# Kernel tuning notes

Measured on AMD Instinct MI355X. Metric: run time of the kernel, lower is better.

The kernel has to match this reference:

```python
import jax, jax.numpy as jnp
import numpy as np

N_NODES = 50000


def gcn_conv(x, W, b, src, dst, n_nodes):
    """PyG GCNConv: add self-loops, symmetric norm, linear, scatter-add, bias."""
    h = x @ W  # [N, out]
    # degree with self-loops: deg[i] = 1 + (# edges with dst == i)
    deg = 1.0 + jax.ops.segment_sum(jnp.ones_like(dst, dtype=h.dtype), dst,
                                    num_segments=n_nodes)
    dinv = jax.lax.rsqrt(deg)  # deg^{-1/2}
    # per-edge norm for non-self-loop edges
    norm = dinv[src] * dinv[dst]  # [E]
    agg = jax.ops.segment_sum(h[src] * norm[:, None], dst,
                              num_segments=n_nodes)
    # self-loop contribution: dinv[i]*dinv[i]*h[i] = h[i]/deg[i]
    agg = agg + h * (dinv * dinv)[:, None]
    return agg + b


def setup_inputs() -> dict:
    key = jax.random.key(0)
    ks = jax.random.split(key, 6)
    x = jax.random.normal(ks[0], (N_NODES, 512), dtype=jnp.float32)
    edge_index = jax.random.randint(ks[1], (2, 800000), 0, N_NODES,
                                    dtype=jnp.int64)
    W1 = jax.random.normal(ks[2], (512, 256), dtype=jnp.float32) * (512 ** -0.5)
    b1 = jnp.zeros((256,), dtype=jnp.float32)
    W2 = jax.random.normal(ks[3], (256, 256), dtype=jnp.float32) * (256 ** -0.5)
    b2 = jnp.zeros((256,), dtype=jnp.float32)
    W3 = jax.random.normal(ks[4], (256, 64), dtype=jnp.float32) * (256 ** -0.5)
    b3 = jnp.zeros((64,), dtype=jnp.float32)
    return {"x": x, "edge_index": edge_index, "W1": W1, "b1": b1,
            "W2": W2, "b2": b2, "W3": W3, "b3": b3}


def reference(x, edge_index, W1, b1, W2, b2, W3, b3):
    src, dst = edge_index[0], edge_index[1]
    n = x.shape[0]
    h = gcn_conv(x, W1, b1, src, dst, n)
    h = jax.nn.relu(h)  # dropout is a no-op in eval mode
    h = gcn_conv(h, W2, b2, src, dst, n)
    h = jax.nn.relu(h)
    h = gcn_conv(h, W3, b3, src, dst, n)
    # faithful to the original: softmax then log_softmax
    h = jax.nn.softmax(h, axis=1)
    return jax.nn.log_softmax(h, axis=1)
```

## Files before the change

kernel.cpp:

```cpp
#include <hip/hip_runtime.h>
#include <cstdint>
#include <cstddef>

typedef float  f32x4  __attribute__((ext_vector_type(4)));
typedef __bf16 bf16x8 __attribute__((ext_vector_type(8)));
typedef unsigned short u16x8 __attribute__((ext_vector_type(8)));
typedef unsigned short u16x4 __attribute__((ext_vector_type(4)));

__device__ __forceinline__ unsigned short f2bf(float f) {
  union { float f; unsigned int u; } v; v.f = f;
  unsigned int r = v.u + 0x7fffu + ((v.u >> 16) & 1u);
  return (unsigned short)(r >> 16);
}
__device__ __forceinline__ float bf2f(unsigned short h) {
  union { unsigned int u; float f; } v; v.u = ((unsigned int)h) << 16;
  return v.f;
}

__device__ __forceinline__ void async_copy16(const unsigned short* g, unsigned short* l) {
  __builtin_amdgcn_global_load_lds(
      (const __attribute__((address_space(1))) unsigned int*)g,
      (__attribute__((address_space(3))) unsigned int*)l, 16, 0, 0);
}

#define NN 50000
#define MPAD 50048
#define SCAN_BLOCKS 196

#define XB_BLOCKS 12512
#define ZB_BLOCKS 196
#define WB_BLOCKS 104

__global__ __launch_bounds__(256) void gcn_prep_k(
    const float* __restrict__ X, unsigned short* __restrict__ xb,
    int* __restrict__ cnt,
    const float* __restrict__ W1, const float* __restrict__ W2,
    const float* __restrict__ W3,
    unsigned short* __restrict__ W1T, unsigned short* __restrict__ W2T,
    unsigned short* __restrict__ W3T) {
  int b = blockIdx.x;
  if (b < XB_BLOCKS) {
    int idx8 = (b * 256 + threadIdx.x) * 8;
    int row = idx8 >> 9;
    u16x8 o;
    if (row < NN) {
      const float* s = &X[idx8];
      float4 v0 = *(const float4*)s;
      float4 v1 = *(const float4*)(s + 4);
      o[0] = f2bf(v0.x); o[1] = f2bf(v0.y); o[2] = f2bf(v0.z); o[3] = f2bf(v0.w);
      o[4] = f2bf(v1.x); o[5] = f2bf(v1.y); o[6] = f2bf(v1.z); o[7] = f2bf(v1.w);
    } else {
      o = u16x8{0, 0, 0, 0, 0, 0, 0, 0};
    }
    *(u16x8*)&xb[idx8] = o;
  } else if (b < XB_BLOCKS + ZB_BLOCKS) {
    int i = (b - XB_BLOCKS) * 256 + threadIdx.x;
    if (i < NN) cnt[i] = 0;
  } else if (b < XB_BLOCKS + ZB_BLOCKS + WB_BLOCKS) {
    int idx8 = ((b - XB_BLOCKS - ZB_BLOCKS) * 256 + threadIdx.x) * 8;
    u16x8 o;
    if (idx8 < 131072) {
#pragma unroll
      for (int j = 0; j < 8; j++) {
        int idx = idx8 + j; int n = idx >> 9, k = idx & 511;
        o[j] = f2bf(W1[(size_t)k * 256 + n]);
      }
      *(u16x8*)&W1T[idx8] = o;
    } else if (idx8 < 196608) {
      int j0 = idx8 - 131072;
#pragma unroll
      for (int j = 0; j < 8; j++) {
        int idx = j0 + j; int n = idx >> 8, k = idx & 255;
        o[j] = f2bf(W2[(size_t)k * 256 + n]);
      }
      *(u16x8*)&W2T[j0] = o;
    } else if (idx8 < 212992) {
      int j0 = idx8 - 196608;
#pragma unroll
      for (int j = 0; j < 8; j++) {
        int idx = j0 + j; int n = idx >> 8, k = idx & 255;
        o[j] = f2bf(W3[(size_t)k * 64 + n]);
      }
      *(u16x8*)&W3T[j0] = o;
    }
  }
}

__global__ void gcn_count_k(const int* __restrict__ dst, int* __restrict__ cnt, int E) {
  int e = blockIdx.x * 256 + threadIdx.x;
  if (e < E) atomicAdd(&cnt[dst[e]], 1);
}

__global__ __launch_bounds__(256) void gcn_scan_blocks_k(
    const int* __restrict__ cnt, int* __restrict__ blockSum, int nNodes) {
  __shared__ int sw[4];
  int t = threadIdx.x;
  int i = blockIdx.x * 256 + t;
  int v = (i < nNodes) ? cnt[i] : 0;
  for (int off = 32; off > 0; off >>= 1) v += __shfl_down(v, off);
  if ((t & 63) == 0) sw[t >> 6] = v;
  __syncthreads();
  if (t == 0) blockSum[blockIdx.x] = sw[0] + sw[1] + sw[2] + sw[3];
}

__global__ __launch_bounds__(256) void gcn_scan_tops_k(
    int* __restrict__ blockSum, int nBlocks) {
  __shared__ int sb[256];
  int t = threadIdx.x;
  int v = (t < nBlocks) ? blockSum[t] : 0;
  sb[t] = v;
  __syncthreads();
  for (int off = 1; off < 256; off <<= 1) {
    int x = (t >= off) ? sb[t - off] : 0;
    __syncthreads();
    sb[t] += x;
    __syncthreads();
  }
  if (t < nBlocks) blockSum[t] = sb[t] - v;
}

__global__ __launch_bounds__(256) void gcn_scan_final_k(
    const int* __restrict__ cnt, const int* __restrict__ blockSum,
    int* __restrict__ rs, int* __restrict__ cur, float* __restrict__ dinv,
    int nNodes, int E) {
  __shared__ int sb[256];
  int t = threadIdx.x;
  int i = blockIdx.x * 256 + t;
  int v = (i < nNodes) ? cnt[i] : 0;
  sb[t] = v;
  __syncthreads();
  for (int off = 1; off < 256; off <<= 1) {
    int x = (t >= off) ? sb[t - off] : 0;
    __syncthreads();
    sb[t] += x;
    __syncthreads();
  }
  if (i < nNodes) {
    int off = blockSum[blockIdx.x] + sb[t] - v;
    rs[i] = off; cur[i] = off;
    dinv[i] = rsqrtf(1.0f + (float)v);
  }
  if (i == 0) rs[nNodes] = E;
}

__global__ void gcn_scatter_k(const int* __restrict__ src, const int* __restrict__ dst,
                              int* __restrict__ cur, const float* __restrict__ dinv,
                              int2* __restrict__ e2, int E) {
  int e = blockIdx.x * 256 + threadIdx.x;
  if (e < E) {
    int d = dst[e];
    int s = src[e];
    int p = atomicAdd(&cur[d], 1);
    int2 v; v.x = s; v.y = __float_as_int(dinv[s] * dinv[d]);
    e2[p] = v;
  }
}

template<int BN, int WTN>
__global__ __launch_bounds__(256) void gcn_gemm_k(
    const unsigned short* __restrict__ A,
    const unsigned short* __restrict__ Bt,
    unsigned short* __restrict__ C,
    int K, int N) {
  __shared__ __align__(16) unsigned short lds_a[128 * 32];
  __shared__ __align__(16) unsigned short lds_b[BN * 32];
  const int t = threadIdx.x;
  const int wave = t >> 6, lane = t & 63;
  const int wr = wave >> 1, wc = wave & 1;
  const int quad = lane >> 4, lrow = lane & 15;
  const int m0 = blockIdx.x * 128;
  const int n0 = blockIdx.y * BN;

  f32x4 acc[4][WTN] = {};

  for (int k0 = 0; k0 < K; k0 += 32) {
    __syncthreads();
    for (int q = t; q < 512; q += 256) {
      int r = q >> 2, c = (q & 3) * 8;
      async_copy16(&A[(size_t)(m0 + r) * K + k0 + c], &lds_a[q * 8]);
    }
    for (int q = t; q < BN * 4; q += 256) {
      int r = q >> 2, c = (q & 3) * 8;
      async_copy16(&Bt[(size_t)(n0 + r) * K + k0 + c], &lds_b[q * 8]);
    }
    __syncthreads();
    bf16x8 af[4], bfr[WTN];
#pragma unroll
    for (int mt = 0; mt < 4; mt++)
      af[mt] = *(const bf16x8*)&lds_a[(wr * 64 + mt * 16 + lrow) * 32 + quad * 8];
#pragma unroll
    for (int nt = 0; nt < WTN; nt++)
      bfr[nt] = *(const bf16x8*)&lds_b[(wc * (BN / 2) + nt * 16 + lrow) * 32 + quad * 8];
#pragma unroll
    for (int mt = 0; mt < 4; mt++)
#pragma unroll
      for (int nt = 0; nt < WTN; nt++)
        acc[mt][nt] = __builtin_amdgcn_mfma_f32_16x16x32_bf16(af[mt], bfr[nt], acc[mt][nt], 0, 0, 0);
  }

#pragma unroll
  for (int mt = 0; mt < 4; mt++)
#pragma unroll
    for (int nt = 0; nt < WTN; nt++)
#pragma unroll
      for (int r = 0; r < 4; r++) {
        int row = m0 + wr * 64 + mt * 16 + quad * 4 + r;
        int col = n0 + wc * (BN / 2) + nt * 16 + lrow;
        C[(size_t)row * N + col] = f2bf(acc[mt][nt][r]);
      }
}

template<int D>
__global__ __launch_bounds__(256) void gcn_agg_relu_k(
    const unsigned short* __restrict__ h, const int* __restrict__ rs,
    const int2* __restrict__ e2, const float* __restrict__ dinv,
    const float* __restrict__ bias, unsigned short* __restrict__ out, int nNodes) {
  int wave = threadIdx.x >> 6, lane = threadIdx.x & 63;
  int i = blockIdx.x * 4 + wave;
  if (i >= nNodes) return;
  int half = lane >> 5, sub = lane & 31;
  int f0 = sub * 8;
  float di = dinv[i];
  u16x8 hv = *(const u16x8*)&h[(size_t)i * D + f0];
  float wself = (half == 0) ? di * di : 0.0f;
  float acc[8];
#pragma unroll
  for (int j = 0; j < 8; j++) acc[j] = bf2f(hv[j]) * wself;

  int e0 = rs[i], e1 = rs[i + 1];
  int nIter = (e1 - e0 + 7) >> 3;
  int e = e0 + half;
  for (int k = 0; k < nIter; k++) {
    int idx[4]; float w[4];
#pragma unroll
    for (int u = 0; u < 4; u++) {
      int ee = e + 2 * u;
      bool v = ee < e1;
      int2 pr = e2[v ? ee : e0];
      idx[u] = v ? pr.x : i;
      w[u] = v ? __int_as_float(pr.y) : 0.0f;
    }
    u16x8 r0 = *(const u16x8*)&h[(size_t)idx[0] * D + f0];
    u16x8 r1 = *(const u16x8*)&h[(size_t)idx[1] * D + f0];
    u16x8 r2 = *(const u16x8*)&h[(size_t)idx[2] * D + f0];
    u16x8 r3 = *(const u16x8*)&h[(size_t)idx[3] * D + f0];
#pragma unroll
    for (int j = 0; j < 8; j++)
      acc[j] += bf2f(r0[j]) * w[0] + bf2f(r1[j]) * w[1] +
                bf2f(r2[j]) * w[2] + bf2f(r3[j]) * w[3];
    e += 8;
  }
#pragma unroll
  for (int j = 0; j < 8; j++) acc[j] += __shfl_xor(acc[j], 32);
  if (half == 0) {
    u16x8 o;
#pragma unroll
    for (int j = 0; j < 8; j++) {
      float r = acc[j] + bias[f0 + j];
      o[j] = f2bf(r > 0.0f ? r : 0.0f);
    }
    *(u16x8*)&out[(size_t)i * D + f0] = o;
  }
}

__global__ __launch_bounds__(256) void gcn_agg_final_k(
    const unsigned short* __restrict__ h, const int* __restrict__ rs,
    const int2* __restrict__ e2, const float* __restrict__ dinv,
    const float* __restrict__ bias, float* __restrict__ out, int nNodes) {
  int wave = threadIdx.x >> 6, lane = threadIdx.x & 63;
  int i = blockIdx.x * 4 + wave;
  if (i >= nNodes) return;
  int qtr = lane >> 4, sub = lane & 15;
  int f0 = sub * 4;
  float di = dinv[i];
  u16x4 hv = *(const u16x4*)&h[(size_t)i * 64 + f0];
  float wself = (qtr == 0) ? di * di : 0.0f;
  float acc[4];
#pragma unroll
  for (int j = 0; j < 4; j++) acc[j] = bf2f(hv[j]) * wself;

  int e0 = rs[i], e1 = rs[i + 1];
  int nIter = (e1 - e0 + 7) >> 3;
  int e = e0 + qtr;
  for (int k = 0; k < nIter; k++) {
    int idx[2]; float w[2];
#pragma unroll
    for (int u = 0; u < 2; u++) {
      int ee = e + 4 * u;
      bool v = ee < e1;
      int2 pr = e2[v ? ee : e0];
      idx[u] = v ? pr.x : i;
      w[u] = v ? __int_as_float(pr.y) : 0.0f;
    }
    u16x4 r0 = *(const u16x4*)&h[(size_t)idx[0] * 64 + f0];
    u16x4 r1 = *(const u16x4*)&h[(size_t)idx[1] * 64 + f0];
#pragma unroll
    for (int j = 0; j < 4; j++)
      acc[j] += bf2f(r0[j]) * w[0] + bf2f(r1[j]) * w[1];
    e += 8;
  }
#pragma unroll
  for (int j = 0; j < 4; j++) {
    acc[j] += __shfl_xor(acc[j], 16);
    acc[j] += __shfl_xor(acc[j], 32);
    acc[j] += bias[f0 + j];
  }
  float m = fmaxf(fmaxf(acc[0], acc[1]), fmaxf(acc[2], acc[3]));
#pragma unroll
  for (int off = 8; off > 0; off >>= 1) m = fmaxf(m, __shfl_xor(m, off));
  float ex[4], s = 0.0f;
#pragma unroll
  for (int j = 0; j < 4; j++) { ex[j] = __expf(acc[j] - m); s += ex[j]; }
#pragma unroll
  for (int off = 8; off > 0; off >>= 1) s += __shfl_xor(s, off);
  float rcs = 1.0f / s;
  float p[4], s2 = 0.0f;
#pragma unroll
  for (int j = 0; j < 4; j++) { p[j] = ex[j] * rcs; s2 += __expf(p[j]); }
#pragma unroll
  for (int off = 8; off > 0; off >>= 1) s2 += __shfl_xor(s2, off);
  float ls = __logf(s2);
  if (qtr == 0) {
    float4 o; o.x = p[0] - ls; o.y = p[1] - ls; o.z = p[2] - ls; o.w = p[3] - ls;
    *(float4*)&out[(size_t)i * 64 + f0] = o;
  }
}

extern "C" void kernel_launch(void* const* d_in, const int* in_sizes, int n_in,
                              void* d_out, int out_size, void* d_ws, size_t ws_size,
                              hipStream_t stream) {
  const float* x    = (const float*)d_in[0];
  const int*   eidx = (const int*)d_in[1];
  const float* W1   = (const float*)d_in[2];
  const float* b1   = (const float*)d_in[3];
  const float* W2   = (const float*)d_in[4];
  const float* b2   = (const float*)d_in[5];
  const float* W3   = (const float*)d_in[6];
  const float* b3   = (const float*)d_in[7];
  float* out = (float*)d_out;

  const int E = in_sizes[1] / 2;
  const int* src = eidx;
  const int* dst = eidx + E;

  char* p = (char*)d_ws;
  auto alloc = [&](size_t bytes) -> void* {
    void* r = (void*)p;
    p += (bytes + 255) & ~(size_t)255;
    return r;
  };
  unsigned short* xb  = (unsigned short*)alloc((size_t)MPAD * 512 * 2);
  unsigned short* hb  = (unsigned short*)alloc((size_t)MPAD * 256 * 2);
  unsigned short* ab  = (unsigned short*)alloc((size_t)MPAD * 256 * 2);
  unsigned short* h3  = (unsigned short*)alloc((size_t)MPAD * 64 * 2);
  unsigned short* W1T = (unsigned short*)alloc((size_t)256 * 512 * 2);
  unsigned short* W2T = (unsigned short*)alloc((size_t)256 * 256 * 2);
  unsigned short* W3T = (unsigned short*)alloc((size_t)64 * 256 * 2);
  int*   cnt  = (int*)alloc((size_t)NN * 4);
  int*   rs   = (int*)alloc((size_t)(NN + 1) * 4);
  int*   cur  = (int*)alloc((size_t)NN * 4);
  float* dinv = (float*)alloc((size_t)NN * 4);
  int2*  e2   = (int2*)alloc((size_t)E * 8);
  int*   bsum = (int*)alloc((size_t)SCAN_BLOCKS * 4);

  gcn_prep_k<<<XB_BLOCKS + ZB_BLOCKS + WB_BLOCKS, 256, 0, stream>>>(
      x, xb, cnt, W1, W2, W3, W1T, W2T, W3T);
  gcn_count_k<<<(E + 255) / 256, 256, 0, stream>>>(dst, cnt, E);
  gcn_scan_blocks_k<<<SCAN_BLOCKS, 256, 0, stream>>>(cnt, bsum, NN);
  gcn_scan_tops_k<<<1, 256, 0, stream>>>(bsum, SCAN_BLOCKS);
  gcn_scan_final_k<<<SCAN_BLOCKS, 256, 0, stream>>>(cnt, bsum, rs, cur, dinv, NN, E);
  gcn_scatter_k<<<(E + 255) / 256, 256, 0, stream>>>(src, dst, cur, dinv, e2, E);

  const int MB = MPAD / 128;
  gcn_gemm_k<128, 4><<<dim3(MB, 2), 256, 0, stream>>>(xb, W1T, hb, 512, 256);
  gcn_agg_relu_k<256><<<(NN + 3) / 4, 256, 0, stream>>>(hb, rs, e2, dinv, b1, ab, NN);
  gcn_gemm_k<128, 4><<<dim3(MB, 2), 256, 0, stream>>>(ab, W2T, hb, 256, 256);
  gcn_agg_relu_k<256><<<(NN + 3) / 4, 256, 0, stream>>>(hb, rs, e2, dinv, b2, ab, NN);
  gcn_gemm_k<64, 2><<<dim3(MB, 1), 256, 0, stream>>>(ab, W3T, h3, 256, 64);
  gcn_agg_final_k<<<(NN + 3) / 4, 256, 0, stream>>>(h3, rs, e2, dinv, b3, out, NN);

  (void)n_in; (void)out_size; (void)ws_size;
}
```

Before: 466.6 us.

## Store GEMM outputs as FP8 to halve gather traffic in aggregation

```diff
diff --git a/kernel.cpp b/kernel.cpp
--- a/kernel.cpp
+++ b/kernel.cpp
@@ -3,6 +3,7 @@
 #include <cstddef>
 
 typedef float  f32x4  __attribute__((ext_vector_type(4)));
+typedef float  f32x2  __attribute__((ext_vector_type(2)));
 typedef __bf16 bf16x8 __attribute__((ext_vector_type(8)));
 typedef unsigned short u16x8 __attribute__((ext_vector_type(8)));
 typedef unsigned short u16x4 __attribute__((ext_vector_type(4)));
@@ -16,6 +17,22 @@
   union { unsigned int u; float f; } v; v.u = ((unsigned int)h) << 16;
   return v.f;
 }
+__device__ __forceinline__ unsigned char f2fp8(float f) {
+  return (unsigned char)(__builtin_amdgcn_cvt_pk_fp8_f32(f, f, 0, false) & 0xff);
+}
+__device__ __forceinline__ void fp8x8_to_f32(uint2 d, float* f) {
+  f32x2 a = __builtin_amdgcn_cvt_pk_f32_fp8((int)d.x, false);
+  f32x2 b = __builtin_amdgcn_cvt_pk_f32_fp8((int)d.x, true);
+  f32x2 c = __builtin_amdgcn_cvt_pk_f32_fp8((int)d.y, false);
+  f32x2 e = __builtin_amdgcn_cvt_pk_f32_fp8((int)d.y, true);
+  f[0] = a.x; f[1] = a.y; f[2] = b.x; f[3] = b.y;
+  f[4] = c.x; f[5] = c.y; f[6] = e.x; f[7] = e.y;
+}
+__device__ __forceinline__ void fp8x4_to_f32(unsigned int d, float* f) {
+  f32x2 a = __builtin_amdgcn_cvt_pk_f32_fp8((int)d, false);
+  f32x2 b = __builtin_amdgcn_cvt_pk_f32_fp8((int)d, true);
+  f[0] = a.x; f[1] = a.y; f[2] = b.x; f[3] = b.y;
+}
 
 __device__ __forceinline__ void async_copy16(const unsigned short* g, unsigned short* l) {
   __builtin_amdgcn_global_load_lds(
@@ -28,16 +45,20 @@
 #define SCAN_BLOCKS 196
 
 #define XB_BLOCKS 12512
-#define ZB_BLOCKS 196
 #define WB_BLOCKS 104
+
+__global__ void gcn_zero_k(int* __restrict__ p, int n) {
+  int i = blockIdx.x * 256 + threadIdx.x;
+  if (i < n) p[i] = 0;
+}
 
 __global__ __launch_bounds__(256) void gcn_prep_k(
     const float* __restrict__ X, unsigned short* __restrict__ xb,
-    int* __restrict__ cnt,
     const float* __restrict__ W1, const float* __restrict__ W2,
     const float* __restrict__ W3,
     unsigned short* __restrict__ W1T, unsigned short* __restrict__ W2T,
-    unsigned short* __restrict__ W3T) {
+    unsigned short* __restrict__ W3T,
+    const int* __restrict__ dst, int* __restrict__ cnt, int E) {
   int b = blockIdx.x;
   if (b < XB_BLOCKS) {
     int idx8 = (b * 256 + threadIdx.x) * 8;
@@ -53,11 +74,8 @@
       o = u16x8{0, 0, 0, 0, 0, 0, 0, 0};
     }
     *(u16x8*)&xb[idx8] = o;
-  } else if (b < XB_BLOCKS + ZB_BLOCKS) {
-    int i = (b - XB_BLOCKS) * 256 + threadIdx.x;
-    if (i < NN) cnt[i] = 0;
-  } else if (b < XB_BLOCKS + ZB_BLOCKS + WB_BLOCKS) {
-    int idx8 = ((b - XB_BLOCKS - ZB_BLOCKS) * 256 + threadIdx.x) * 8;
+  } else if (b < XB_BLOCKS + WB_BLOCKS) {
+    int idx8 = ((b - XB_BLOCKS) * 256 + threadIdx.x) * 8;
     u16x8 o;
     if (idx8 < 131072) {
 #pragma unroll
@@ -83,12 +101,10 @@
       }
       *(u16x8*)&W3T[j0] = o;
     }
-  }
-}
-
-__global__ void gcn_count_k(const int* __restrict__ dst, int* __restrict__ cnt, int E) {
-  int e = blockIdx.x * 256 + threadIdx.x;
-  if (e < E) atomicAdd(&cnt[dst[e]], 1);
+  } else {
+    int e = (b - XB_BLOCKS - WB_BLOCKS) * 256 + threadIdx.x;
+    if (e < E) atomicAdd(&cnt[dst[e]], 1);
+  }
 }
 
 __global__ __launch_bounds__(256) void gcn_scan_blocks_k(
@@ -160,7 +176,7 @@
 __global__ __launch_bounds__(256) void gcn_gemm_k(
     const unsigned short* __restrict__ A,
     const unsigned short* __restrict__ Bt,
-    unsigned short* __restrict__ C,
+    unsigned char* __restrict__ C8,
     int K, int N) {
   __shared__ __align__(16) unsigned short lds_a[128 * 32];
   __shared__ __align__(16) unsigned short lds_b[BN * 32];
@@ -206,13 +222,13 @@
       for (int r = 0; r < 4; r++) {
         int row = m0 + wr * 64 + mt * 16 + quad * 4 + r;
         int col = n0 + wc * (BN / 2) + nt * 16 + lrow;
-        C[(size_t)row * N + col] = f2bf(acc[mt][nt][r]);
+        C8[(size_t)row * N + col] = f2fp8(acc[mt][nt][r]);
       }
 }
 
 template<int D>
 __global__ __launch_bounds__(256) void gcn_agg_relu_k(
-    const unsigned short* __restrict__ h, const int* __restrict__ rs,
+    const unsigned char* __restrict__ h8, const int* __restrict__ rs,
     const int2* __restrict__ e2, const float* __restrict__ dinv,
     const float* __restrict__ bias, unsigned short* __restrict__ out, int nNodes) {
   int wave = threadIdx.x >> 6, lane = threadIdx.x & 63;
@@ -221,11 +237,13 @@
   int half = lane >> 5, sub = lane & 31;
   int f0 = sub * 8;
   float di = dinv[i];
-  u16x8 hv = *(const u16x8*)&h[(size_t)i * D + f0];
+  uint2 dsel = *(const uint2*)&h8[(size_t)i * D + f0];
+  float sv[8];
+  fp8x8_to_f32(dsel, sv);
   float wself = (half == 0) ? di * di : 0.0f;
   float acc[8];
 #pragma unroll
-  for (int j = 0; j < 8; j++) acc[j] = bf2f(hv[j]) * wself;
+  for (int j = 0; j < 8; j++) acc[j] = sv[j] * wself;
 
   int e0 = rs[i], e1 = rs[i + 1];
   int nIter = (e1 - e0 + 7) >> 3;
@@ -240,14 +258,16 @@
       idx[u] = v ? pr.x : i;
       w[u] = v ? __int_as_float(pr.y) : 0.0f;
     }
-    u16x8 r0 = *(const u16x8*)&h[(size_t)idx[0] * D + f0];
-    u16x8 r1 = *(const u16x8*)&h[(size_t)idx[1] * D + f0];
-    u16x8 r2 = *(const u16x8*)&h[(size_t)idx[2] * D + f0];
-    u16x8 r3 = *(const u16x8*)&h[(size_t)idx[3] * D + f0];
+    uint2 d0 = *(const uint2*)&h8[(size_t)idx[0] * D + f0];
+    uint2 d1 = *(const uint2*)&h8[(size_t)idx[1] * D + f0];
+    uint2 d2 = *(const uint2*)&h8[(size_t)idx[2] * D + f0];
+    uint2 d3 = *(const uint2*)&h8[(size_t)idx[3] * D + f0];
+    float r0[8], r1[8], r2[8], r3[8];
+    fp8x8_to_f32(d0, r0); fp8x8_to_f32(d1, r1);
+    fp8x8_to_f32(d2, r2); fp8x8_to_f32(d3, r3);
 #pragma unroll
     for (int j = 0; j < 8; j++)
-      acc[j] += bf2f(r0[j]) * w[0] + bf2f(r1[j]) * w[1] +
-                bf2f(r2[j]) * w[2] + bf2f(r3[j]) * w[3];
+      acc[j] += r0[j] * w[0] + r1[j] * w[1] + r2[j] * w[2] + r3[j] * w[3];
     e += 8;
   }
 #pragma unroll
@@ -264,7 +284,7 @@
 }
 
 __global__ __launch_bounds__(256) void gcn_agg_final_k(
-    const unsigned short* __restrict__ h, const int* __restrict__ rs,
+    const unsigned char* __restrict__ h8, const int* __restrict__ rs,
     const int2* __restrict__ e2, const float* __restrict__ dinv,
     const float* __restrict__ bias, float* __restrict__ out, int nNodes) {
   int wave = threadIdx.x >> 6, lane = threadIdx.x & 63;
@@ -273,11 +293,13 @@
   int qtr = lane >> 4, sub = lane & 15;
   int f0 = sub * 4;
   float di = dinv[i];
-  u16x4 hv = *(const u16x4*)&h[(size_t)i * 64 + f0];
+  unsigned int dself = *(const unsigned int*)&h8[(size_t)i * 64 + f0];
+  float sv[4];
+  fp8x4_to_f32(dself, sv);
   float wself = (qtr == 0) ? di * di : 0.0f;
   float acc[4];
 #pragma unroll
-  for (int j = 0; j < 4; j++) acc[j] = bf2f(hv[j]) * wself;
+  for (int j = 0; j < 4; j++) acc[j] = sv[j] * wself;
 
   int e0 = rs[i], e1 = rs[i + 1];
   int nIter = (e1 - e0 + 7) >> 3;
@@ -292,11 +314,13 @@
       idx[u] = v ? pr.x : i;
       w[u] = v ? __int_as_float(pr.y) : 0.0f;
     }
-    u16x4 r0 = *(const u16x4*)&h[(size_t)idx[0] * 64 + f0];
-    u16x4 r1 = *(const u16x4*)&h[(size_t)idx[1] * 64 + f0];
+    unsigned int d0 = *(const unsigned int*)&h8[(size_t)idx[0] * 64 + f0];
+    unsigned int d1 = *(const unsigned int*)&h8[(size_t)idx[1] * 64 + f0];
+    float r0[4], r1[4];
+    fp8x4_to_f32(d0, r0); fp8x4_to_f32(d1, r1);
 #pragma unroll
     for (int j = 0; j < 4; j++)
-      acc[j] += bf2f(r0[j]) * w[0] + bf2f(r1[j]) * w[1];
+      acc[j] += r0[j] * w[0] + r1[j] * w[1];
     e += 8;
   }
 #pragma unroll
@@ -350,9 +374,9 @@
     return r;
   };
   unsigned short* xb  = (unsigned short*)alloc((size_t)MPAD * 512 * 2);
-  unsigned short* hb  = (unsigned short*)alloc((size_t)MPAD * 256 * 2);
+  unsigned char*  h8  = (unsigned char*)alloc((size_t)MPAD * 256);
   unsigned short* ab  = (unsigned short*)alloc((size_t)MPAD * 256 * 2);
-  unsigned short* h3  = (unsigned short*)alloc((size_t)MPAD * 64 * 2);
+  unsigned char*  h83 = (unsigned char*)alloc((size_t)MPAD * 64);
   unsigned short* W1T = (unsigned short*)alloc((size_t)256 * 512 * 2);
   unsigned short* W2T = (unsigned short*)alloc((size_t)256 * 256 * 2);
   unsigned short* W3T = (unsigned short*)alloc((size_t)64 * 256 * 2);
@@ -363,21 +387,22 @@
   int2*  e2   = (int2*)alloc((size_t)E * 8);
   int*   bsum = (int*)alloc((size_t)SCAN_BLOCKS * 4);
 
-  gcn_prep_k<<<XB_BLOCKS + ZB_BLOCKS + WB_BLOCKS, 256, 0, stream>>>(
-      x, xb, cnt, W1, W2, W3, W1T, W2T, W3T);
-  gcn_count_k<<<(E + 255) / 256, 256, 0, stream>>>(dst, cnt, E);
+  const int EB = (E + 255) / 256;
+  gcn_zero_k<<<SCAN_BLOCKS, 256, 0, stream>>>(cnt, NN);
+  gcn_prep_k<<<XB_BLOCKS + WB_BLOCKS + EB, 256, 0, stream>>>(
+      x, xb, W1, W2, W3, W1T, W2T, W3T, dst, cnt, E);
   gcn_scan_blocks_k<<<SCAN_BLOCKS, 256, 0, stream>>>(cnt, bsum, NN);
   gcn_scan_tops_k<<<1, 256, 0, stream>>>(bsum, SCAN_BLOCKS);
   gcn_scan_final_k<<<SCAN_BLOCKS, 256, 0, stream>>>(cnt, bsum, rs, cur, dinv, NN, E);
-  gcn_scatter_k<<<(E + 255) / 256, 256, 0, stream>>>(src, dst, cur, dinv, e2, E);
+  gcn_scatter_k<<<EB, 256, 0, stream>>>(src, dst, cur, dinv, e2, E);
 
   const int MB = MPAD / 128;
-  gcn_gemm_k<128, 4><<<dim3(MB, 2), 256, 0, stream>>>(xb, W1T, hb, 512, 256);
-  gcn_agg_relu_k<256><<<(NN + 3) / 4, 256, 0, stream>>>(hb, rs, e2, dinv, b1, ab, NN);
-  gcn_gemm_k<128, 4><<<dim3(MB, 2), 256, 0, stream>>>(ab, W2T, hb, 256, 256);
-  gcn_agg_relu_k<256><<<(NN + 3) / 4, 256, 0, stream>>>(hb, rs, e2, dinv, b2, ab, NN);
-  gcn_gemm_k<64, 2><<<dim3(MB, 1), 256, 0, stream>>>(ab, W3T, h3, 256, 64);
-  gcn_agg_final_k<<<(NN + 3) / 4, 256, 0, stream>>>(h3, rs, e2, dinv, b3, out, NN);
+  gcn_gemm_k<128, 4><<<dim3(MB, 2), 256, 0, stream>>>(xb, W1T, h8, 512, 256);
+  gcn_agg_relu_k<256><<<(NN + 3) / 4, 256, 0, stream>>>(h8, rs, e2, dinv, b1, ab, NN);
+  gcn_gemm_k<128, 4><<<dim3(MB, 2), 256, 0, stream>>>(ab, W2T, h8, 256, 256);
+  gcn_agg_relu_k<256><<<(NN + 3) / 4, 256, 0, stream>>>(h8, rs, e2, dinv, b2, ab, NN);
+  gcn_gemm_k<64, 2><<<dim3(MB, 1), 256, 0, stream>>>(ab, W3T, h83, 256, 64);
+  gcn_agg_final_k<<<(NN + 3) / 4, 256, 0, stream>>>(h83, rs, e2, dinv, b3, out, NN);
 
   (void)n_in; (void)out_size; (void)ws_size;
 }
```

Result: faster. 418.6 us (-10.3%).
